# Kernel tuning notes

Hardware: AMD Instinct MI355X
Metric: run time of the kernel (lower is better)

## Reference

```python
import jax, jax.numpy as jnp
import numpy as np

NA = 4
NC = 60


def setup_inputs() -> dict:
    key = jax.random.key(0)
    k1, k2 = jax.random.split(key)
    bs, nG = 8, 128
    p = jax.random.normal(k1, (bs, NA * (5 + NC), nG, nG), dtype=jnp.float32)
    # anchor (w, h) in pixels; positive, realistic scale
    anchors = jax.random.uniform(k2, (NA, 2), dtype=jnp.float32) * 100.0 + 10.0
    return {"p": p, "anchors": anchors, "img_dim": 1024}


def reference(p, anchors, img_dim):
    bs = p.shape[0]
    nG = p.shape[2]
    nA = anchors.shape[0]
    nC = p.shape[1] // nA - 5
    stride = jnp.float32(img_dim) / nG

    # [bs, nA, nG, nG, 5+nC]
    p = p.reshape(bs, nA, 5 + nC, nG, nG).transpose(0, 1, 3, 4, 2)

    x = jax.nn.sigmoid(p[..., 0])
    y = jax.nn.sigmoid(p[..., 1])
    w = jax.nn.sigmoid(p[..., 2])
    h = jax.nn.sigmoid(p[..., 3])
    pred_conf = p[..., 4]
    pred_cls = p[..., 5:]

    grid = jnp.arange(nG, dtype=jnp.float32)
    grid_x = grid[None, None, None, :]   # broadcast over rows
    grid_y = grid[None, None, :, None]   # broadcast over cols
    scaled = anchors / stride            # [nA, 2]
    anchor_w = scaled[:, 0][None, :, None, None]
    anchor_h = scaled[:, 1][None, :, None, None]

    width = (w * 2.0) ** 2 * anchor_w
    height = (h * 2.0) ** 2 * anchor_h

    # [bs, nA, nG, nG, 4]
    pred_boxes = jnp.stack((x + grid_x, y + grid_y, width, height), axis=-1)

    output = jnp.concatenate(
        (
            pred_boxes.reshape(bs, -1, 4) * stride,
            jax.nn.sigmoid(pred_conf).reshape(bs, -1, 1),
            pred_cls.reshape(bs, -1, nC),
        ),
        axis=-1,
    )
    return output
```

## Files before the change

kernel.cpp:

```cpp
#include <hip/hip_runtime.h>


namespace {
constexpr int kNA  = 4;
constexpr int kNC  = 60;
constexpr int kNCH = kNC + 5;
constexpr int kNG  = 128;
constexpr int kThreads = 512;
constexpr int kRow  = kNG * kNG;
constexpr int kItems = kNCH * (kNG / 4);
constexpr int kIter  = (kItems + kThreads - 1) / kThreads;
}

__global__ __launch_bounds__(kThreads, 8)
void yolo_head_kernel(const float* __restrict__ p,
                      const float* __restrict__ anchors,
                      const int* __restrict__ img_dim,
                      float* __restrict__ out)
{
    __shared__ float tile[kNG * kNCH];

    const int blk = blockIdx.x;
    const int gy  = blk & (kNG - 1);
    const int ba  = blk >> 7;
    const int a   = ba & (kNA - 1);
    const int b   = ba >> 2;

    const float stride = (float)img_dim[0] / (float)kNG;
    const float aw4 = 4.0f * anchors[2 * a];
    const float ah4 = 4.0f * anchors[2 * a + 1];
    const float gyf = (float)gy;

    const int t = threadIdx.x;
    const float* __restrict__ pin =
        p + (((size_t)b * (kNA * kNCH) + (size_t)a * kNCH) * kNG + gy) * kNG;

    float4 v[kIter];
    #pragma unroll
    for (int i = 0; i < kIter; ++i) {
        const int l = t + i * kThreads;
        if (l < kItems)
            v[i] = *reinterpret_cast<const float4*>(
                pin + (size_t)(l >> 5) * kRow + (size_t)(l & 31) * 4);
    }

    #pragma unroll
    for (int i = 0; i < kIter; ++i) {
        const int l = t + i * kThreads;
        if (l >= kItems) continue;
        const int c = l >> 5;
        const int s = (l & 31) * 4;
        float r[4] = {v[i].x, v[i].y, v[i].z, v[i].w};
        if (c < 5) {
            #pragma unroll
            for (int j = 0; j < 4; ++j) {
                const float sg = 1.0f / (1.0f + expf(-r[j]));
                if (c == 0)      r[j] = (sg + (float)(s + j)) * stride;
                else if (c == 1) r[j] = (sg + gyf) * stride;
                else if (c == 2) r[j] = sg * sg * aw4;
                else if (c == 3) r[j] = sg * sg * ah4;
                else             r[j] = sg;
            }
        }
        #pragma unroll
        for (int j = 0; j < 4; ++j)
            tile[(s + j) * kNCH + c] = r[j];
    }

    __syncthreads();

    float4* __restrict__ op = reinterpret_cast<float4*>(
        out + (size_t)(((b * kNA + a) * kNG + gy) * kNG) * kNCH);
    const float4* tp = reinterpret_cast<const float4*>(tile);
    #pragma unroll
    for (int i = 0; i < kIter; ++i) {
        const int l = t + i * kThreads;
        if (l < kItems) op[l] = tp[l];
    }
}

extern "C" void kernel_launch(void* const* d_in, const int* in_sizes, int n_in,
                              void* d_out, int out_size, void* d_ws, size_t ws_size,
                              hipStream_t stream)
{
    const float* p       = (const float*)d_in[0];
    const float* anchors = (const float*)d_in[1];
    const int*   img_dim = (const int*)d_in[2];
    float* out = (float*)d_out;

    const int bs = in_sizes[0] / (kNA * kNCH * kNG * kNG);
    const int nblocks = bs * kNA * kNG;
    yolo_head_kernel<<<nblocks, kThreads, 0, stream>>>(p, anchors, img_dim, out);
}
```

Before: 237.2 us.

## Load input directly to LDS via global_load_lds and process two rows per block

Each block now handles two grid rows (256 pixels) instead of one. The input channels go straight from global memory into an LDS staging tile with the async global_load_lds builtin, and the transpose is done through a second LDS tile with 4-channel gathers per thread. The goal is to cut register pressure and VGPR round trips for loads, and to halve block count. In exchange it uses about 133 KB of dynamic LDS per block, which limits occupancy to one block per CU. That removes overlap between blocks, and load latency is fully exposed before the barrier.

```diff
diff --git a/kernel.cpp b/kernel.cpp
--- a/kernel.cpp
+++ b/kernel.cpp
@@ -1,81 +1,100 @@
 #include <hip/hip_runtime.h>
+#include <cstdint>
 
 
 namespace {
-constexpr int kNA  = 4;
-constexpr int kNC  = 60;
-constexpr int kNCH = kNC + 5;
-constexpr int kNG  = 128;
+constexpr int kNA      = 4;
+constexpr int kNCH     = 65;
+constexpr int kNG      = 128;
 constexpr int kThreads = 512;
-constexpr int kRow  = kNG * kNG;
-constexpr int kItems = kNCH * (kNG / 4);
-constexpr int kIter  = (kItems + kThreads - 1) / kThreads;
+constexpr int kPix     = 256;
+constexpr int kTileF   = kNCH * kPix;
+constexpr int kLdsBytes= 2 * kTileF * 4;
 }
 
-__global__ __launch_bounds__(kThreads, 8)
+#define AS1 __attribute__((address_space(1)))
+#define AS3 __attribute__((address_space(3)))
+
+__device__ __forceinline__ float sigm(float v) { return 1.0f / (1.0f + expf(-v)); }
+
+__global__ __launch_bounds__(kThreads, 1)
 void yolo_head_kernel(const float* __restrict__ p,
                       const float* __restrict__ anchors,
                       const int* __restrict__ img_dim,
                       float* __restrict__ out)
 {
-    __shared__ float tile[kNG * kNCH];
+    extern __shared__ float lds[];
+    float* in_t  = lds;
+    float* out_t = lds + kTileF;
 
-    const int blk = blockIdx.x;
-    const int gy  = blk & (kNG - 1);
-    const int ba  = blk >> 7;
+    const int bid = blockIdx.x;
+    const int gyp = bid & 63;
+    const int ba  = bid >> 6;
     const int a   = ba & (kNA - 1);
     const int b   = ba >> 2;
+    const int gy0 = gyp * 2;
+
+    const int t    = threadIdx.x;
+    const int wv   = t >> 6;
+    const int lane = t & 63;
+
+    const float* base = p + ((size_t)(b * (kNA*kNCH) + a * kNCH) * kNG + gy0) * kNG;
+    #pragma unroll
+    for (int i = 0; i < 9; ++i) {
+        const int c = wv + i * 8;
+        if (c < kNCH) {
+            const float* src = base + (size_t)c * (kNG * kNG) + lane * 4;
+            __builtin_amdgcn_global_load_lds((const AS1 uint32_t*)src,
+                                             (AS3 uint32_t*)(in_t + c * kPix),
+                                             16, 0, 0);
+        }
+    }
 
     const float stride = (float)img_dim[0] / (float)kNG;
     const float aw4 = 4.0f * anchors[2 * a];
     const float ah4 = 4.0f * anchors[2 * a + 1];
-    const float gyf = (float)gy;
 
-    const int t = threadIdx.x;
-    const float* __restrict__ pin =
-        p + (((size_t)b * (kNA * kNCH) + (size_t)a * kNCH) * kNG + gy) * kNG;
-
-    float4 v[kIter];
-    #pragma unroll
-    for (int i = 0; i < kIter; ++i) {
-        const int l = t + i * kThreads;
-        if (l < kItems)
-            v[i] = *reinterpret_cast<const float4*>(
-                pin + (size_t)(l >> 5) * kRow + (size_t)(l & 31) * 4);
-    }
+    __syncthreads();
 
     #pragma unroll
-    for (int i = 0; i < kIter; ++i) {
+    for (int i = 0; i < 9; ++i) {
         const int l = t + i * kThreads;
-        if (l >= kItems) continue;
-        const int c = l >> 5;
-        const int s = (l & 31) * 4;
-        float r[4] = {v[i].x, v[i].y, v[i].z, v[i].w};
-        if (c < 5) {
-            #pragma unroll
-            for (int j = 0; j < 4; ++j) {
-                const float sg = 1.0f / (1.0f + expf(-r[j]));
-                if (c == 0)      r[j] = (sg + (float)(s + j)) * stride;
-                else if (c == 1) r[j] = (sg + gyf) * stride;
-                else if (c == 2) r[j] = sg * sg * aw4;
-                else if (c == 3) r[j] = sg * sg * ah4;
-                else             r[j] = sg;
+        if (l < kPix * 17) {
+            const int s = l & (kPix - 1);
+            const int q = l >> 8;
+            if (q < 16) {
+                const int c0 = 4 * q;
+                float r0 = in_t[(c0 + 0) * kPix + s];
+                float r1 = in_t[(c0 + 1) * kPix + s];
+                float r2 = in_t[(c0 + 2) * kPix + s];
+                float r3 = in_t[(c0 + 3) * kPix + s];
+                if (q == 0) {
+                    const float gx  = (float)(s & (kNG - 1));
+                    const float gyf = (float)(gy0 + (s >> 7));
+                    r0 = (sigm(r0) + gx) * stride;
+                    r1 = (sigm(r1) + gyf) * stride;
+                    float sg = sigm(r2); r2 = sg * sg * aw4;
+                    sg = sigm(r3);       r3 = sg * sg * ah4;
+                } else if (q == 1) {
+                    r0 = sigm(r0);
+                }
+                float* o = out_t + s * kNCH + c0;
+                o[0] = r0; o[1] = r1; o[2] = r2; o[3] = r3;
+            } else {
+                out_t[s * kNCH + 64] = in_t[64 * kPix + s];
             }
         }
-        #pragma unroll
-        for (int j = 0; j < 4; ++j)
-            tile[(s + j) * kNCH + c] = r[j];
     }
 
     __syncthreads();
 
     float4* __restrict__ op = reinterpret_cast<float4*>(
-        out + (size_t)(((b * kNA + a) * kNG + gy) * kNG) * kNCH);
-    const float4* tp = reinterpret_cast<const float4*>(tile);
+        out + (size_t)(ba * (kNG * kNG) + gy0 * kNG) * kNCH);
+    const float4* tp = reinterpret_cast<const float4*>(out_t);
     #pragma unroll
-    for (int i = 0; i < kIter; ++i) {
-        const int l = t + i * kThreads;
-        if (l < kItems) op[l] = tp[l];
+    for (int i = 0; i < 9; ++i) {
+        const int f = t + i * kThreads;
+        if (f < kTileF / 4) op[f] = tp[f];
     }
 }
 
@@ -88,7 +107,10 @@
     const int*   img_dim = (const int*)d_in[2];
     float* out = (float*)d_out;
 
+    (void)hipFuncSetAttribute((const void*)yolo_head_kernel,
+                              hipFuncAttributeMaxDynamicSharedMemorySize, kLdsBytes);
+
     const int bs = in_sizes[0] / (kNA * kNCH * kNG * kNG);
-    const int nblocks = bs * kNA * kNG;
-    yolo_head_kernel<<<nblocks, kThreads, 0, stream>>>(p, anchors, img_dim, out);
+    const int nblocks = bs * kNA * (kNG / 2);
+    yolo_head_kernel<<<nblocks, kThreads, kLdsBytes, stream>>>(p, anchors, img_dim, out);
 }
```

Measured after the change: 236.5 us. Within noise of the previous version (-0.3%).
